# Performance work log

Hardware: AMD Instinct MI355X
Metric: run time of the kernel (lower is better)

Reference implementation:

```python
import jax, jax.numpy as jnp
import numpy as np

SMPL_PARENTS = [-1, 0, 0, 0, 1, 2, 3, 4, 5, 6, 7, 8, 9, 9, 9, 12, 13, 14, 16, 17, 18, 19, 20, 21]
J = 24  # SMPL_NR_JOINTS


def _adj_norm():
    # kinematic tree edges, to_undirected + add_self_loops, row-normalized -> mean over in-neighbors
    A = np.zeros((J, J), np.float32)
    for c, p in enumerate(SMPL_PARENTS):
        if p >= 0:
            A[c, p] = 1.0
            A[p, c] = 1.0
    A += np.eye(J, dtype=np.float32)
    return A / A.sum(axis=1, keepdims=True)

A_NORM = jnp.asarray(_adj_norm())


def _forward(src, tgt, enc_W, enc_b, sage_Wl, sage_bl, sage_Wr, gate_w, gate_b, dec_W, dec_b):
    N, T_src, _ = src.shape
    T_out = tgt.shape[1]
    D = enc_W.shape[1]

    def enc(frame):  # [N, J*3] -> [N, J, D]
        x = frame.reshape(N, J, -1)
        return jax.nn.relu(x @ enc_W + enc_b)

    def sage(i, z):  # PyG SAGEConv: lin_l(mean_{j in N(i)} x_j) + lin_r(x_i)
        agg = jnp.einsum('jk,nkd->njd', A_NORM, z)
        return agg @ sage_Wl[i] + sage_bl[i] + z @ sage_Wr[i]

    def cell(x, h, c):
        I = jax.nn.sigmoid(sage(0, x) + sage(1, h) + gate_w[0] * c + gate_b[0])
        F = jax.nn.sigmoid(sage(2, x) + sage(3, h) + gate_w[1] * c + gate_b[1])
        T = jnp.tanh(sage(4, x) + sage(5, h) + gate_b[2])
        c_new = F * c + I * T
        O = jax.nn.sigmoid(sage(6, x) + sage(7, h) + gate_w[2] * c_new + gate_b[3])
        h_new = O * jnp.tanh(c_new)
        return O, h_new, c_new

    zero = jnp.zeros((N, J, D), src.dtype)
    # warm-up over the last 12 src frames; first step re-encodes with fresh (h, c)=0
    out, h, c = cell(enc(src[:, T_src - 12]), zero, zero)

    def warm_step(carry, _):
        o, h, c = carry
        return cell(o, h, c), None

    (out, h, c), _ = jax.lax.scan(warm_step, (out, h, c), None, length=11)

    out0, h, c = cell(enc(tgt[:, 0]), h, c)

    def dec_step(carry, _):
        o, h, c = carry
        o, h, c = cell(o, h, c)
        return (o, h, c), o

    _, rest = jax.lax.scan(dec_step, (out0, h, c), None, length=T_out - 1)
    outs = jnp.concatenate([out0[None], rest], axis=0)  # [T_out, N, J, D]
    outs = outs.transpose(1, 0, 2, 3).reshape(N, T_out, J * D)
    return outs @ dec_W + dec_b  # [N, T_out, J*3]


def setup_inputs():
    key = jax.random.key(0)
    ks = jax.random.split(key, 8)
    N, T_src, T_out = 1024, 16, 12
    A_in, D = 3, 64
    s = 1.0 / np.sqrt(D)
    return {
        'src': jax.random.normal(ks[0], (N, T_src, J * A_in), jnp.float32),
        'tgt': jax.random.normal(ks[1], (N, T_out, J * A_in), jnp.float32),
        'enc_W': jax.random.normal(ks[2], (A_in, D), jnp.float32) * (1.0 / np.sqrt(A_in)),
        'enc_b': jnp.zeros((D,), jnp.float32),
        'sage_Wl': jax.random.normal(ks[3], (8, D, D), jnp.float32) * s,
        'sage_bl': jnp.zeros((8, D), jnp.float32),
        'sage_Wr': jax.random.normal(ks[4], (8, D, D), jnp.float32) * s,
        'gate_w': jax.random.normal(ks[5], (3, 1, D), jnp.float32) * s,
        'gate_b': jnp.zeros((4, 1, D), jnp.float32),
        'dec_W': jax.random.normal(ks[6], (J * D, J * A_in), jnp.float32) * (1.0 / np.sqrt(J * D)),
        'dec_b': jnp.zeros((J * A_in,), jnp.float32),
    }


def reference(src, tgt, enc_W, enc_b, sage_Wl, sage_bl, sage_Wr, gate_w, gate_b, dec_W, dec_b):
    return _forward(src, tgt, enc_W, enc_b, sage_Wl, sage_bl, sage_Wr, gate_w, gate_b, dec_W, dec_b)
```

## Files before the change

kernel.cpp:

```cpp
#include <hip/hip_runtime.h>


typedef _Float16 f16x8 __attribute__((ext_vector_type(8)));
typedef float f32x16 __attribute__((ext_vector_type(16)));

__constant__ int c_nbr2[24][5] = {
  {0,1,2,3,24},  {1,0,4,24,24}, {2,0,5,24,24}, {3,0,6,24,24},
  {4,1,7,24,24}, {5,2,8,24,24}, {6,3,9,24,24}, {7,4,10,24,24},
  {8,5,11,24,24},{9,6,12,13,14},{10,7,24,24,24},{11,8,24,24,24},
  {12,9,15,24,24},{13,9,16,24,24},{14,9,17,24,24},{15,12,24,24,24},
  {16,13,18,24,24},{17,14,19,24,24},{18,16,20,24,24},{19,17,21,24,24},
  {20,18,22,24,24},{21,19,23,24,24},{22,20,24,24,24},{23,21,24,24,24}
};
__constant__ float c_invdeg[24] = {
  0.25f, 1.f/3.f, 1.f/3.f, 1.f/3.f, 1.f/3.f, 1.f/3.f, 1.f/3.f, 1.f/3.f,
  1.f/3.f, 0.2f, 0.5f, 0.5f, 1.f/3.f, 1.f/3.f, 1.f/3.f, 0.5f,
  1.f/3.f, 1.f/3.f, 1.f/3.f, 1.f/3.f, 1.f/3.f, 1.f/3.f, 0.5f, 0.5f
};

__device__ __forceinline__ unsigned short f2h(float f) {
  _Float16 h = (_Float16)f;
  return __builtin_bit_cast(unsigned short, h);
}
__device__ __forceinline__ unsigned pk2h(float a, float b) {
  return (unsigned)f2h(a) | ((unsigned)f2h(b) << 16);
}
__device__ __forceinline__ unsigned pkrtz(float lo, float hi) {
  unsigned r;
  asm("v_cvt_pkrtz_f16_f32 %0, %1, %2" : "=v"(r) : "v"(lo), "v"(hi));
  return r;
}
__device__ __forceinline__ float h2f_lo(unsigned u) {
  return (float)__builtin_bit_cast(_Float16, (unsigned short)(u & 0xffff));
}
__device__ __forceinline__ float h2f_hi(unsigned u) {
  return (float)__builtin_bit_cast(_Float16, (unsigned short)(u >> 16));
}
__device__ __forceinline__ float sigm_(float x) {
  return __builtin_amdgcn_rcpf(1.0f + __expf(-x));
}
__device__ __forceinline__ float tanh_(float x) {
  return 1.0f - 2.0f * __builtin_amdgcn_rcpf(1.0f + __expf(2.0f * x));
}

__global__ void prep4_kernel(const float* __restrict__ sWl, const float* __restrict__ sbl,
                             const float* __restrict__ sWr, const float* __restrict__ gb,
                             const float* __restrict__ dW,
                             unsigned short* __restrict__ Wfrag,
                             float* __restrict__ biasv,
                             unsigned short* __restrict__ Bdec)
{
  int id = blockIdx.x * 256 + threadIdx.x;
  if (id < 65536) {
    int i = id & 7, l = (id >> 3) & 63, t = (id >> 9) & 15, mt = id >> 13;
    int m32 = l & 31;
    int g = m32 & 3, d = mt * 8 + (m32 >> 2);
    int k = t * 16 + ((l >> 5) << 3) + i;
    int q = k >> 6, kk = k & 63;
    const float* Ws = (q & 1) ? sWr : sWl;
    Wfrag[id] = f2h(Ws[((2 * g + (q >> 1)) * 64 + kk) * 64 + d]);
  } else if (id < 65792) {
    int c = id - 65536;
    int mt = c >> 5, m32 = c & 31;
    int g = m32 & 3, d = mt * 8 + (m32 >> 2);
    biasv[c] = sbl[(2 * g) * 64 + d] + sbl[(2 * g + 1) * 64 + d] + gb[g * 64 + d];
  } else {
    int p = id - 65792;
    int i = p & 7, l = (p >> 3) & 63;
    int rem = p >> 9;
    int nt = rem / 96, t = rem - nt * 96;
    int e = nt * 32 + (l & 31);
    int k = t * 16 + ((l >> 5) << 3) + i;
    Bdec[p] = (e < 72) ? f2h(dW[k * 72 + e]) : (unsigned short)0;
  }
}

__global__ __launch_bounds__(512, 4) void mono9_kernel(
    const float* __restrict__ src, const float* __restrict__ tgt,
    const float* __restrict__ encW, const float* __restrict__ encb,
    const float* __restrict__ gw,
    const unsigned short* __restrict__ Wfrag,
    const float* __restrict__ biasv,
    unsigned short* __restrict__ obuf)
{
  __shared__ __align__(16) unsigned short AGG[2][8 * 64 * 8];
  __shared__ __align__(16) unsigned short XH[2][2][8 * 64 * 8];

  const int tid = threadIdx.x;
  const int n2 = blockIdx.x * 2;
  const int w = tid >> 6, l = tid & 63;
  const int l31 = l & 31, hi = l >> 5;

  f16x8 W[16];
  {
    const f16x8* p0 = reinterpret_cast<const f16x8*>(Wfrag) + (w * 16) * 64 + l;
    #pragma unroll
    for (int t = 0; t < 16; ++t) W[t] = p0[t * 64];
  }
  unsigned bias_u[8];
  #pragma unroll
  for (int p = 0; p < 8; ++p) {
    int r0 = 2 * p, r1 = 2 * p + 1;
    int m0 = (r0 & 3) + 8 * (r0 >> 2) + 4 * hi;
    int m1 = (r1 & 3) + 8 * (r1 >> 2) + 4 * hi;
    bias_u[p] = pk2h(biasv[w * 32 + m0], biasv[w * 32 + m1]);
  }
  float gwv[12];
  #pragma unroll
  for (int g = 0; g < 3; ++g)
    #pragma unroll
    for (int u = 0; u < 4; ++u)
      gwv[g * 4 + u] = gw[g * 64 + w * 8 + 2 * u + hi];

  float creg[8];
  #pragma unroll
  for (int i = 0; i < 8; ++i) creg[i] = 0.0f;

  {
    uint4 z = make_uint4(0, 0, 0, 0);
    uint4* xz = reinterpret_cast<uint4*>(&XH[0][0][0]);
    #pragma unroll
    for (int i = 0; i < 4; ++i) xz[tid + i * 512] = z;
    uint4* az = reinterpret_cast<uint4*>(&AGG[0][0]);
    #pragma unroll
    for (int i = 0; i < 2; ++i) az[tid + i * 512] = z;
  }

  auto enc_to_x = [&](const float* f0, const float* f1, int buf) {
    #pragma unroll
    for (int ii = 0; ii < 6; ++ii) {
      int idx = tid + ii * 512;
      int e = (idx >= 1536) ? 1 : 0;
      int r = idx - e * 1536;
      int j = r >> 6, d = r & 63;
      const float* f = (e ? f1 : f0) + j * 3;
      float v = encb[d] + f[0] * encW[d] + f[1] * encW[64 + d] + f[2] * encW[128 + d];
      XH[buf][e][((d >> 4) * 64 + j + ((d >> 3) & 1) * 32) * 8 + (d & 7)] =
          f2h(fmaxf(v, 0.0f));
    }
  };

  auto agg_job = [&](int jb, int e, int srcbuf) {
    int sec = (jb >= 192) ? 1 : 0;
    int r2 = jb - sec * 192;
    int ch = (r2 * 683) >> 14;
    int Mrow = r2 - ch * 24;
    int sbase = (sec * 4 + (ch >> 1)) * 64 + ((ch & 1) << 5);
    const unsigned short* xh = &XH[srcbuf][e][0];
    f16x8 s0 = *reinterpret_cast<const f16x8*>(xh + (sbase + c_nbr2[Mrow][0]) * 8);
    #pragma unroll
    for (int m = 1; m < 5; ++m) {
      s0 += *reinterpret_cast<const f16x8*>(xh + (sbase + c_nbr2[Mrow][m]) * 8);
    }
    s0 *= (_Float16)c_invdeg[Mrow];
    *reinterpret_cast<f16x8*>(&AGG[e][0] + (sbase + Mrow) * 8) = s0;
  };

  int cur = 0;

  enc_to_x(src + ((size_t)n2 * 16 + 4) * 72,
           src + ((size_t)(n2 + 1) * 16 + 4) * 72, 0);
  __syncthreads();
  if (tid < 384) agg_job(tid, 0, 0);
  __syncthreads();

  auto phase = [&](int eg, int ea, int aggsrc, int step) {
    const unsigned short* aggb = &AGG[eg][0];
    const unsigned short* xhb  = &XH[cur][eg][0];
    f32x16 acc;
    #pragma unroll
    for (int p = 0; p < 8; ++p) {
      acc[2 * p]     = h2f_lo(bias_u[p]);
      acc[2 * p + 1] = h2f_hi(bias_u[p]);
    }
    #pragma unroll
    for (int t = 0; t < 4; ++t)
      acc = __builtin_amdgcn_mfma_f32_32x32x16_f16(
          W[t], *reinterpret_cast<const f16x8*>(aggb + (t * 64 + l) * 8), acc, 0, 0, 0);
    #pragma unroll
    for (int t = 0; t < 4; ++t)
      acc = __builtin_amdgcn_mfma_f32_32x32x16_f16(
          W[4 + t], *reinterpret_cast<const f16x8*>(xhb + (t * 64 + l) * 8), acc, 0, 0, 0);
    #pragma unroll
    for (int t = 0; t < 4; ++t)
      acc = __builtin_amdgcn_mfma_f32_32x32x16_f16(
          W[8 + t], *reinterpret_cast<const f16x8*>(aggb + ((4 + t) * 64 + l) * 8), acc, 0, 0, 0);
    #pragma unroll
    for (int t = 0; t < 4; ++t)
      acc = __builtin_amdgcn_mfma_f32_32x32x16_f16(
          W[12 + t], *reinterpret_cast<const f16x8*>(xhb + ((4 + t) * 64 + l) * 8), acc, 0, 0, 0);

    if (tid < 384) agg_job(tid, ea, aggsrc);

    if (l31 < 24) {
      unsigned short* xw = &XH[cur ^ 1][eg][0];
      const int wb = ((w >> 1) * 64 + l31 + ((w & 1) << 5)) * 8;
      #pragma unroll
      for (int u = 0; u < 4; ++u) {
        float cv = creg[eg * 4 + u];
        float I = sigm_(acc[4 * u + 0] + gwv[u] * cv);
        float F = sigm_(acc[4 * u + 1] + gwv[4 + u] * cv);
        float T = tanh_(acc[4 * u + 2]);
        float cn = F * cv + I * T;
        float O = sigm_(acc[4 * u + 3] + gwv[8 + u] * cn);
        float h = O * tanh_(cn);
        creg[eg * 4 + u] = cn;
        unsigned oh = pkrtz(O, h);
        int d7 = 2 * u + hi;
        xw[wb + d7]        = (unsigned short)oh;
        xw[2048 + wb + d7] = (unsigned short)(oh >> 16);
        if (step >= 12)
          obuf[(size_t)((n2 + eg) * 12 + step - 12) * 1536 + l31 * 64 + w * 8 + d7] =
              (unsigned short)oh;
      }
    }
  };

  #pragma unroll 1
  for (int step = 0; step < 24; ++step) {
    if (step == 12) {
      enc_to_x(tgt + (size_t)n2 * 864, tgt + (size_t)(n2 + 1) * 864, cur);
      __syncthreads();
      if (tid < 384) agg_job(tid, 0, cur);
      __syncthreads();
    }
    phase(0, 1, cur, step);
    __syncthreads();
    phase(1, 0, cur ^ 1, step);
    __syncthreads();
    cur ^= 1;
  }
}

__global__ __launch_bounds__(256) void dec4_kernel(
    const unsigned short* __restrict__ obuf,
    const unsigned short* __restrict__ Bdec,
    const float* __restrict__ db,
    float* __restrict__ out)
{
  __shared__ float part[4 * 3 * 64 * 16];
  const int tid = threadIdx.x;
  const int w = tid >> 6, l = tid & 63;
  const int l31 = l & 31, hi = l >> 5;
  const int r0 = blockIdx.x * 32;

  f32x16 a0, a1, a2;
  #pragma unroll
  for (int r = 0; r < 16; ++r) { a0[r] = 0.f; a1[r] = 0.f; a2[r] = 0.f; }

  const unsigned short* Ap = obuf + (size_t)(r0 + l31) * 1536 + hi * 8;
  #pragma unroll 4
  for (int tt = 0; tt < 24; ++tt) {
    int kt = w * 24 + tt;
    f16x8 av = *reinterpret_cast<const f16x8*>(Ap + kt * 16);
    f16x8 b0 = *reinterpret_cast<const f16x8*>(Bdec + ((0 * 96 + kt) * 64 + l) * 8);
    f16x8 b1 = *reinterpret_cast<const f16x8*>(Bdec + ((1 * 96 + kt) * 64 + l) * 8);
    f16x8 b2 = *reinterpret_cast<const f16x8*>(Bdec + ((2 * 96 + kt) * 64 + l) * 8);
    a0 = __builtin_amdgcn_mfma_f32_32x32x16_f16(av, b0, a0, 0, 0, 0);
    a1 = __builtin_amdgcn_mfma_f32_32x32x16_f16(av, b1, a1, 0, 0, 0);
    a2 = __builtin_amdgcn_mfma_f32_32x32x16_f16(av, b2, a2, 0, 0, 0);
  }
  #pragma unroll
  for (int r = 0; r < 16; ++r) {
    part[((w * 3 + 0) * 64 + l) * 16 + r] = a0[r];
    part[((w * 3 + 1) * 64 + l) * 16 + r] = a1[r];
    part[((w * 3 + 2) * 64 + l) * 16 + r] = a2[r];
  }
  __syncthreads();

  int row = tid >> 3;
  int hi2 = (row >> 2) & 1;
  int rr = 4 * (row >> 3) + (row & 3);
  #pragma unroll
  for (int ei = 0; ei < 12; ++ei) {
    int e = (tid & 7) * 12 + ei;
    if (e < 72) {
      int nt = e >> 5, e32 = e & 31;
      float s = db[e];
      #pragma unroll
      for (int w2 = 0; w2 < 4; ++w2)
        s += part[((w2 * 3 + nt) * 64 + e32 + 32 * hi2) * 16 + rr];
      out[(size_t)(r0 + row) * 72 + e] = s;
    }
  }
}

extern "C" void kernel_launch(void* const* d_in, const int* in_sizes, int n_in,
                              void* d_out, int out_size, void* d_ws, size_t ws_size,
                              hipStream_t stream) {
  const float* src  = (const float*)d_in[0];
  const float* tgt  = (const float*)d_in[1];
  const float* encW = (const float*)d_in[2];
  const float* encb = (const float*)d_in[3];
  const float* sWl  = (const float*)d_in[4];
  const float* sbl  = (const float*)d_in[5];
  const float* sWr  = (const float*)d_in[6];
  const float* gw   = (const float*)d_in[7];
  const float* gb   = (const float*)d_in[8];
  const float* dW   = (const float*)d_in[9];
  const float* db   = (const float*)d_in[10];
  float* out = (float*)d_out;

  unsigned short* obuf  = (unsigned short*)d_ws;
  unsigned short* Wfrag = obuf + (size_t)12288 * 1536;
  unsigned short* Bdec  = Wfrag + 65536;
  float*          biasv = (float*)(Bdec + 147456);

  prep4_kernel<<<833, 256, 0, stream>>>(sWl, sbl, sWr, gb, dW, Wfrag, biasv, Bdec);
  mono9_kernel<<<512, 512, 0, stream>>>(src, tgt, encW, encb, gw, Wfrag, biasv, obuf);
  dec4_kernel<<<384, 256, 0, stream>>>(obuf, Bdec, db, out);
}
```

Measured before the change: 203.7 us.

## Software-pipeline the two LSTM sequences and drop the double-buffered XH

Restructures the recurrent loop so the gate epilogue of one sequence runs after the MFMA GEMM of the other, with aggregation done per wave in place. This removes the XH ping-pong buffer, which halves that shared memory. The weight rows are permuted so each lane owns four contiguous hidden dims, turning scalar 16-bit stores into 64-bit packed stores to LDS and obuf. The risks are the subtle read-after-write ordering on the single XH buffer and extra live accumulator registers.

```diff
diff --git a/kernel.cpp b/kernel.cpp
--- a/kernel.cpp
+++ b/kernel.cpp
@@ -43,7 +43,7 @@
   return 1.0f - 2.0f * __builtin_amdgcn_rcpf(1.0f + __expf(2.0f * x));
 }
 
-__global__ void prep4_kernel(const float* __restrict__ sWl, const float* __restrict__ sbl,
+__global__ void prep5_kernel(const float* __restrict__ sWl, const float* __restrict__ sbl,
                              const float* __restrict__ sWr, const float* __restrict__ gb,
                              const float* __restrict__ dW,
                              unsigned short* __restrict__ Wfrag,
@@ -54,7 +54,8 @@
   if (id < 65536) {
     int i = id & 7, l = (id >> 3) & 63, t = (id >> 9) & 15, mt = id >> 13;
     int m32 = l & 31;
-    int g = m32 & 3, d = mt * 8 + (m32 >> 2);
+    int g = m32 & 3, tq = m32 >> 2;
+    int d = mt * 8 + (tq >> 1) + 4 * (tq & 1);
     int k = t * 16 + ((l >> 5) << 3) + i;
     int q = k >> 6, kk = k & 63;
     const float* Ws = (q & 1) ? sWr : sWl;
@@ -62,7 +63,8 @@
   } else if (id < 65792) {
     int c = id - 65536;
     int mt = c >> 5, m32 = c & 31;
-    int g = m32 & 3, d = mt * 8 + (m32 >> 2);
+    int g = m32 & 3, tq = m32 >> 2;
+    int d = mt * 8 + (tq >> 1) + 4 * (tq & 1);
     biasv[c] = sbl[(2 * g) * 64 + d] + sbl[(2 * g + 1) * 64 + d] + gb[g * 64 + d];
   } else {
     int p = id - 65792;
@@ -75,7 +77,7 @@
   }
 }
 
-__global__ __launch_bounds__(512, 4) void mono9_kernel(
+__global__ __launch_bounds__(512, 4) void mono10_kernel(
     const float* __restrict__ src, const float* __restrict__ tgt,
     const float* __restrict__ encW, const float* __restrict__ encb,
     const float* __restrict__ gw,
@@ -84,7 +86,7 @@
     unsigned short* __restrict__ obuf)
 {
   __shared__ __align__(16) unsigned short AGG[2][8 * 64 * 8];
-  __shared__ __align__(16) unsigned short XH[2][2][8 * 64 * 8];
+  __shared__ __align__(16) unsigned short XH[2][8 * 64 * 8];
 
   const int tid = threadIdx.x;
   const int n2 = blockIdx.x * 2;
@@ -110,7 +112,7 @@
   for (int g = 0; g < 3; ++g)
     #pragma unroll
     for (int u = 0; u < 4; ++u)
-      gwv[g * 4 + u] = gw[g * 64 + w * 8 + 2 * u + hi];
+      gwv[g * 4 + u] = gw[g * 64 + w * 8 + 4 * hi + u];
 
   float creg[8];
   #pragma unroll
@@ -118,15 +120,11 @@
 
   {
     uint4 z = make_uint4(0, 0, 0, 0);
-    uint4* xz = reinterpret_cast<uint4*>(&XH[0][0][0]);
-    #pragma unroll
-    for (int i = 0; i < 4; ++i) xz[tid + i * 512] = z;
-    uint4* az = reinterpret_cast<uint4*>(&AGG[0][0]);
-    #pragma unroll
-    for (int i = 0; i < 2; ++i) az[tid + i * 512] = z;
-  }
-
-  auto enc_to_x = [&](const float* f0, const float* f1, int buf) {
+    uint4* xz = reinterpret_cast<uint4*>(&XH[0][0]);
+    xz[tid] = z; xz[tid + 512] = z;
+  }
+
+  auto enc_to_x = [&](const float* f0, const float* f1) {
     #pragma unroll
     for (int ii = 0; ii < 6; ++ii) {
       int idx = tid + ii * 512;
@@ -135,38 +133,29 @@
       int j = r >> 6, d = r & 63;
       const float* f = (e ? f1 : f0) + j * 3;
       float v = encb[d] + f[0] * encW[d] + f[1] * encW[64 + d] + f[2] * encW[128 + d];
-      XH[buf][e][((d >> 4) * 64 + j + ((d >> 3) & 1) * 32) * 8 + (d & 7)] =
+      XH[e][((d >> 4) * 64 + j + ((d >> 3) & 1) * 32) * 8 + (d & 7)] =
           f2h(fmaxf(v, 0.0f));
     }
   };
 
-  auto agg_job = [&](int jb, int e, int srcbuf) {
-    int sec = (jb >= 192) ? 1 : 0;
-    int r2 = jb - sec * 192;
-    int ch = (r2 * 683) >> 14;
-    int Mrow = r2 - ch * 24;
-    int sbase = (sec * 4 + (ch >> 1)) * 64 + ((ch & 1) << 5);
-    const unsigned short* xh = &XH[srcbuf][e][0];
-    f16x8 s0 = *reinterpret_cast<const f16x8*>(xh + (sbase + c_nbr2[Mrow][0]) * 8);
-    #pragma unroll
-    for (int m = 1; m < 5; ++m) {
-      s0 += *reinterpret_cast<const f16x8*>(xh + (sbase + c_nbr2[Mrow][m]) * 8);
-    }
-    s0 *= (_Float16)c_invdeg[Mrow];
-    *reinterpret_cast<f16x8*>(&AGG[e][0] + (sbase + Mrow) * 8) = s0;
+  auto agg_w = [&](int e) {
+    if (l31 < 24) {
+      const int sec = hi;
+      const int Mrow = l31;
+      const int sbase = (sec * 4 + (w >> 1)) * 64 + ((w & 1) << 5);
+      const unsigned short* xh = &XH[e][0];
+      f16x8 s = *reinterpret_cast<const f16x8*>(xh + (sbase + c_nbr2[Mrow][0]) * 8);
+      #pragma unroll
+      for (int m = 1; m < 5; ++m)
+        s += *reinterpret_cast<const f16x8*>(xh + (sbase + c_nbr2[Mrow][m]) * 8);
+      s *= (_Float16)c_invdeg[Mrow];
+      *reinterpret_cast<f16x8*>(&AGG[e][0] + (sbase + Mrow) * 8) = s;
+    }
   };
 
-  int cur = 0;
-
-  enc_to_x(src + ((size_t)n2 * 16 + 4) * 72,
-           src + ((size_t)(n2 + 1) * 16 + 4) * 72, 0);
-  __syncthreads();
-  if (tid < 384) agg_job(tid, 0, 0);
-  __syncthreads();
-
-  auto phase = [&](int eg, int ea, int aggsrc, int step) {
-    const unsigned short* aggb = &AGG[eg][0];
-    const unsigned short* xhb  = &XH[cur][eg][0];
+  auto gemm = [&](int e) -> f32x16 {
+    const unsigned short* ab = &AGG[e][0];
+    const unsigned short* xb = &XH[e][0];
     f32x16 acc;
     #pragma unroll
     for (int p = 0; p < 8; ++p) {
@@ -176,60 +165,76 @@
     #pragma unroll
     for (int t = 0; t < 4; ++t)
       acc = __builtin_amdgcn_mfma_f32_32x32x16_f16(
-          W[t], *reinterpret_cast<const f16x8*>(aggb + (t * 64 + l) * 8), acc, 0, 0, 0);
+          W[t], *reinterpret_cast<const f16x8*>(ab + (t * 64 + l) * 8), acc, 0, 0, 0);
     #pragma unroll
     for (int t = 0; t < 4; ++t)
       acc = __builtin_amdgcn_mfma_f32_32x32x16_f16(
-          W[4 + t], *reinterpret_cast<const f16x8*>(xhb + (t * 64 + l) * 8), acc, 0, 0, 0);
+          W[4 + t], *reinterpret_cast<const f16x8*>(xb + (t * 64 + l) * 8), acc, 0, 0, 0);
     #pragma unroll
     for (int t = 0; t < 4; ++t)
       acc = __builtin_amdgcn_mfma_f32_32x32x16_f16(
-          W[8 + t], *reinterpret_cast<const f16x8*>(aggb + ((4 + t) * 64 + l) * 8), acc, 0, 0, 0);
+          W[8 + t], *reinterpret_cast<const f16x8*>(ab + ((4 + t) * 64 + l) * 8), acc, 0, 0, 0);
     #pragma unroll
     for (int t = 0; t < 4; ++t)
       acc = __builtin_amdgcn_mfma_f32_32x32x16_f16(
-          W[12 + t], *reinterpret_cast<const f16x8*>(xhb + ((4 + t) * 64 + l) * 8), acc, 0, 0, 0);
-
-    if (tid < 384) agg_job(tid, ea, aggsrc);
-
+          W[12 + t], *reinterpret_cast<const f16x8*>(xb + ((4 + t) * 64 + l) * 8), acc, 0, 0, 0);
+    return acc;
+  };
+
+  auto epi = [&](const f32x16& acc, int e, int step, bool write_x) {
     if (l31 < 24) {
-      unsigned short* xw = &XH[cur ^ 1][eg][0];
-      const int wb = ((w >> 1) * 64 + l31 + ((w & 1) << 5)) * 8;
+      float Ov[4], Hv[4];
       #pragma unroll
       for (int u = 0; u < 4; ++u) {
-        float cv = creg[eg * 4 + u];
+        float cv = creg[e * 4 + u];
         float I = sigm_(acc[4 * u + 0] + gwv[u] * cv);
         float F = sigm_(acc[4 * u + 1] + gwv[4 + u] * cv);
         float T = tanh_(acc[4 * u + 2]);
         float cn = F * cv + I * T;
         float O = sigm_(acc[4 * u + 3] + gwv[8 + u] * cn);
-        float h = O * tanh_(cn);
-        creg[eg * 4 + u] = cn;
-        unsigned oh = pkrtz(O, h);
-        int d7 = 2 * u + hi;
-        xw[wb + d7]        = (unsigned short)oh;
-        xw[2048 + wb + d7] = (unsigned short)(oh >> 16);
-        if (step >= 12)
-          obuf[(size_t)((n2 + eg) * 12 + step - 12) * 1536 + l31 * 64 + w * 8 + d7] =
-              (unsigned short)oh;
+        Ov[u] = O;
+        Hv[u] = O * tanh_(cn);
+        creg[e * 4 + u] = cn;
       }
+      uint2 ou, hu;
+      ou.x = pkrtz(Ov[0], Ov[1]); ou.y = pkrtz(Ov[2], Ov[3]);
+      hu.x = pkrtz(Hv[0], Hv[1]); hu.y = pkrtz(Hv[2], Hv[3]);
+      unsigned short* xh = &XH[e][0];
+      const int base = (((w >> 1) * 64 + l31 + ((w & 1) << 5)) << 3) + 4 * hi;
+      if (write_x) *reinterpret_cast<uint2*>(xh + base) = ou;
+      *reinterpret_cast<uint2*>(xh + 2048 + base) = hu;
+      if (step >= 12)
+        *reinterpret_cast<uint2*>(
+            obuf + (size_t)((n2 + e) * 12 + step - 12) * 1536 + l31 * 64 + w * 8 + 4 * hi) = ou;
     }
   };
 
+  __syncthreads();
+  enc_to_x(src + ((size_t)n2 * 16 + 4) * 72,
+           src + ((size_t)(n2 + 1) * 16 + 4) * 72);
+  __syncthreads();
+  agg_w(0);
+  __syncthreads();
+
+  f32x16 acc0, acc1;
   #pragma unroll 1
   for (int step = 0; step < 24; ++step) {
     if (step == 12) {
-      enc_to_x(tgt + (size_t)n2 * 864, tgt + (size_t)(n2 + 1) * 864, cur);
+      enc_to_x(tgt + (size_t)n2 * 864, tgt + (size_t)(n2 + 1) * 864);
       __syncthreads();
-      if (tid < 384) agg_job(tid, 0, cur);
+      agg_w(0);
       __syncthreads();
     }
-    phase(0, 1, cur, step);
+    acc0 = gemm(0);
+    if (step > 0) epi(acc1, 1, step - 1, step != 12);
+    agg_w(1);
     __syncthreads();
-    phase(1, 0, cur ^ 1, step);
+    acc1 = gemm(1);
+    epi(acc0, 0, step, true);
+    if (step < 23) agg_w(0);
     __syncthreads();
-    cur ^= 1;
-  }
+  }
+  epi(acc1, 1, 23, false);
 }
 
 __global__ __launch_bounds__(256) void dec4_kernel(
@@ -306,7 +311,7 @@
   unsigned short* Bdec  = Wfrag + 65536;
   float*          biasv = (float*)(Bdec + 147456);
 
-  prep4_kernel<<<833, 256, 0, stream>>>(sWl, sbl, sWr, gb, dW, Wfrag, biasv, Bdec);
-  mono9_kernel<<<512, 512, 0, stream>>>(src, tgt, encW, encb, gw, Wfrag, biasv, obuf);
+  prep5_kernel<<<833, 256, 0, stream>>>(sWl, sbl, sWr, gb, dW, Wfrag, biasv, Bdec);
+  mono10_kernel<<<512, 512, 0, stream>>>(src, tgt, encW, encb, gw, Wfrag, biasv, obuf);
   dec4_kernel<<<384, 256, 0, stream>>>(obuf, Bdec, db, out);
 }
```

After: 251.2 us. 1.23x slower.
